# Performance work log

Measured on AMD Instinct MI355X. Metric: run time of the kernel, lower is better.

Reference implementation:

```python
import jax, jax.numpy as jnp
import numpy as np
from functools import partial

B = 131072          # training_size (batch)
D_IN = 100          # init_shape
H = 50              # neurons
T = 100             # dimTimes
DT = 0.01           # dt = 1/100
GAMMA = 0.05        # gamma = 1/20
I0 = 0.12


def setup_inputs() -> dict:
    key = jax.random.key(0)
    ks = jax.random.split(key, 7)
    s = lambda fan_in: 1.0 / np.sqrt(fan_in)
    return {
        "x": jax.random.normal(ks[0], (B, D_IN), dtype=jnp.float32),
        "W0": jax.random.uniform(ks[1], (H, D_IN), jnp.float32, -s(D_IN), s(D_IN)),
        "b0": jax.random.uniform(ks[2], (H,), jnp.float32, -s(D_IN), s(D_IN)),
        "W1": jax.random.uniform(ks[3], (H, H), jnp.float32, -s(H), s(H)),
        "b1": jax.random.uniform(ks[4], (H,), jnp.float32, -s(H), s(H)),
        "W2": jax.random.uniform(ks[5], (T - 1, H), jnp.float32, -s(H), s(H)),
        "b2": jax.random.uniform(ks[6], (T - 1,), jnp.float32, -s(H), s(H)),
    }


def reference(x, W0, b0, W1, b1, W2, b2):
    # 3-layer MLP: 100 -> 50 -> 50 -> 99
    h = jax.nn.relu(x @ W0.T + b0)
    h = jax.nn.relu(h @ W1.T + b1)
    out = h @ W2.T + b2                      # [B, T-1] growth rates per step

    # Euler recurrence: I[:,k] = I[:,k-1] + dt*(out[:,k-1]*I*(1-I) - gamma*I)
    i0 = jnp.full((x.shape[0],), I0, dtype=out.dtype)

    def step(I_prev, o_k):
        I_new = I_prev + DT * (o_k * I_prev * (1.0 - I_prev) - GAMMA * I_prev)
        return I_new, I_new

    _, I_rest = jax.lax.scan(step, i0, out.T)   # I_rest: [T-1, B]
    I = jnp.concatenate([i0[:, None], I_rest.T], axis=1)  # [B, T]
    return I
```

## Files before the change

kernel.cpp:

```cpp
#include <hip/hip_runtime.h>
#include <stdint.h>

#define BB      131072
#define TT      100
#define DT_C    0.01f
#define GAMMA_C 0.05f
#define I0_C    0.12f

typedef short bf16x8 __attribute__((ext_vector_type(8)));
typedef float f32x4  __attribute__((ext_vector_type(4)));

#define F0_U16  0
#define F1_U16  (16*512)
#define F2_U16  (24*512)
#define NFRAG_U16 (38*512)

__device__ __forceinline__ uint16_t f2bf(float x) {
    uint32_t u = __builtin_bit_cast(uint32_t, x);
    return (uint16_t)((u + 0x7fffu + ((u >> 16) & 1u)) >> 16);
}

__device__ __forceinline__ uint32_t pk2(float a, float b) {
    return (uint32_t)f2bf(a) | ((uint32_t)f2bf(b) << 16);
}

__global__ void pack_kernel(const float* __restrict__ W0, const float* __restrict__ b0,
                            const float* __restrict__ W1, const float* __restrict__ b1,
                            const float* __restrict__ W2, const float* __restrict__ b2,
                            uint16_t* __restrict__ wsu)
{
    const int gid = blockIdx.x * blockDim.x + threadIdx.x;
    const int gsz = gridDim.x * blockDim.x;
    for (int idx = gid; idx < NFRAG_U16; idx += gsz) {
        int f = idx >> 9;
        int r = idx & 511;
        int L = r >> 3, j = r & 7;
        int k8 = ((L >> 4) << 3) + j;
        int n16 = L & 15;
        float v = 0.0f;
        if (f < 16) {
            int kc = f >> 2, nt = f & 3;
            int kk = kc * 32 + k8, nn = nt * 16 + n16;
            if (nn < 50) {
                if (kk < 100) v = W0[nn * 100 + kk];
                else if (kk == 100) v = b0[nn];
            }
        } else if (f < 24) {
            int g = f - 16; int kc = g >> 2, nt = g & 3;
            int kk = kc * 32 + k8, nn = nt * 16 + n16;
            if (nn < 50) {
                if (kk < 50) v = W1[nn * 50 + kk];
                else if (kk == 50) v = b1[nn];
            }
        } else {
            int g = f - 24; int kc = g / 7, nt = g % 7;
            int kk = kc * 32 + k8, nn = nt * 16 + n16;
            if (nn < 99) {
                if (kk < 50) v = DT_C * W2[nn * 50 + kk];
                else if (kk == 50) v = DT_C * b2[nn];
            }
        }
        wsu[idx] = f2bf(v);
    }
}

#define SLAB_F 3712

__global__ __launch_bounds__(256, 2) void net_kernel(
    const float* __restrict__ x,
    const void*  __restrict__ wsv,
    float* __restrict__ out)
{
    __shared__ float lds[4 * SLAB_F];
    const int tid  = threadIdx.x;
    const int wave = tid >> 6, lane = tid & 63;
    const int quad = lane >> 4, l15 = lane & 15;
    float* slabF = lds + wave * SLAB_F;
    uint16_t* h0u = (uint16_t*)slabF;
    uint16_t* h1u = (uint16_t*)slabF + 32 * 88;
    const uint16_t* wsu = (const uint16_t*)wsv;

    const int row0 = (blockIdx.x * 4 + wave) * 32;

    bf16x8 a0[2][4];
    #pragma unroll
    for (int h = 0; h < 2; ++h) {
        const float* xrow = x + (size_t)(row0 + h * 16 + l15) * 100;
        #pragma unroll
        for (int kc = 0; kc < 3; ++kc) {
            f32x4 p = *(const f32x4*)(xrow + kc * 32 + quad * 8);
            f32x4 q = *(const f32x4*)(xrow + kc * 32 + quad * 8 + 4);
            union { bf16x8 v; uint32_t u[4]; } t;
            t.u[0] = pk2(p[0], p[1]); t.u[1] = pk2(p[2], p[3]);
            t.u[2] = pk2(q[0], q[1]); t.u[3] = pk2(q[2], q[3]);
            a0[h][kc] = t.v;
        }
        union { bf16x8 v; uint32_t u[4]; } t;
        t.u[0] = t.u[1] = t.u[2] = t.u[3] = 0u;
        if (quad == 0) {
            f32x4 p = *(const f32x4*)(xrow + 96);
            t.u[0] = pk2(p[0], p[1]); t.u[1] = pk2(p[2], p[3]);
            t.u[2] = 0x00003f80u;
        }
        a0[h][3] = t.v;
    }

    f32x4 acc0[2][4];
    #pragma unroll
    for (int h = 0; h < 2; ++h)
        #pragma unroll
        for (int nt = 0; nt < 4; ++nt) acc0[h][nt] = (f32x4){0.f, 0.f, 0.f, 0.f};
    #pragma unroll
    for (int kc = 0; kc < 4; ++kc) {
        #pragma unroll
        for (int nt = 0; nt < 4; ++nt) {
            bf16x8 b = ((const bf16x8*)(wsu + F0_U16 + (kc * 4 + nt) * 512))[lane];
            acc0[0][nt] = __builtin_amdgcn_mfma_f32_16x16x32_bf16(a0[0][kc], b, acc0[0][nt], 0, 0, 0);
            acc0[1][nt] = __builtin_amdgcn_mfma_f32_16x16x32_bf16(a0[1][kc], b, acc0[1][nt], 0, 0, 0);
        }
    }
    const bool is50 = (l15 == 2);
    #pragma unroll
    for (int h = 0; h < 2; ++h) {
        #pragma unroll
        for (int nt = 0; nt < 4; ++nt) {
            const int n = nt * 16 + l15;
            #pragma unroll
            for (int r2 = 0; r2 < 4; r2 += 2) {
                float v0 = fmaxf(acc0[h][nt][r2], 0.0f);
                float v1 = fmaxf(acc0[h][nt][r2 + 1], 0.0f);
                if (nt == 3 && is50) { v0 = 1.0f; v1 = 1.0f; }
                uint32_t p = pk2(v0, v1);
                const int m = h * 16 + quad * 4 + r2;
                h0u[m * 88 + n]       = (uint16_t)p;
                h0u[(m + 1) * 88 + n] = (uint16_t)(p >> 16);
            }
        }
    }

    bf16x8 a1[2][2];
    #pragma unroll
    for (int h = 0; h < 2; ++h)
        #pragma unroll
        for (int kc = 0; kc < 2; ++kc)
            a1[h][kc] = *(const bf16x8*)(h0u + (h * 16 + l15) * 88 + kc * 32 + quad * 8);

    f32x4 acc1[2][4];
    #pragma unroll
    for (int h = 0; h < 2; ++h)
        #pragma unroll
        for (int nt = 0; nt < 4; ++nt) acc1[h][nt] = (f32x4){0.f, 0.f, 0.f, 0.f};
    #pragma unroll
    for (int kc = 0; kc < 2; ++kc) {
        #pragma unroll
        for (int nt = 0; nt < 4; ++nt) {
            bf16x8 b = ((const bf16x8*)(wsu + F1_U16 + (kc * 4 + nt) * 512))[lane];
            acc1[0][nt] = __builtin_amdgcn_mfma_f32_16x16x32_bf16(a1[0][kc], b, acc1[0][nt], 0, 0, 0);
            acc1[1][nt] = __builtin_amdgcn_mfma_f32_16x16x32_bf16(a1[1][kc], b, acc1[1][nt], 0, 0, 0);
        }
    }
    #pragma unroll
    for (int h = 0; h < 2; ++h) {
        #pragma unroll
        for (int nt = 0; nt < 4; ++nt) {
            const int n = nt * 16 + l15;
            #pragma unroll
            for (int r2 = 0; r2 < 4; r2 += 2) {
                float v0 = fmaxf(acc1[h][nt][r2], 0.0f);
                float v1 = fmaxf(acc1[h][nt][r2 + 1], 0.0f);
                if (nt == 3 && is50) { v0 = 1.0f; v1 = 1.0f; }
                uint32_t p = pk2(v0, v1);
                const int m = h * 16 + quad * 4 + r2;
                h1u[m * 88 + n]       = (uint16_t)p;
                h1u[(m + 1) * 88 + n] = (uint16_t)(p >> 16);
            }
        }
    }

    bf16x8 a2[2][2];
    #pragma unroll
    for (int h = 0; h < 2; ++h)
        #pragma unroll
        for (int kc = 0; kc < 2; ++kc)
            a2[h][kc] = *(const bf16x8*)(h1u + (h * 16 + l15) * 88 + kc * 32 + quad * 8);

    f32x4 acc2[2][7];
    #pragma unroll
    for (int h = 0; h < 2; ++h)
        #pragma unroll
        for (int nt = 0; nt < 7; ++nt) acc2[h][nt] = (f32x4){0.f, 0.f, 0.f, 0.f};
    #pragma unroll
    for (int kc = 0; kc < 2; ++kc) {
        #pragma unroll
        for (int nt = 0; nt < 7; ++nt) {
            bf16x8 b = ((const bf16x8*)(wsu + F2_U16 + (kc * 7 + nt) * 512))[lane];
            acc2[0][nt] = __builtin_amdgcn_mfma_f32_16x16x32_bf16(a2[0][kc], b, acc2[0][nt], 0, 0, 0);
            acc2[1][nt] = __builtin_amdgcn_mfma_f32_16x16x32_bf16(a2[1][kc], b, acc2[1][nt], 0, 0, 0);
        }
    }
    #pragma unroll
    for (int h = 0; h < 2; ++h) {
        #pragma unroll
        for (int nt = 0; nt < 7; ++nt) {
            const int t = nt * 16 + l15;
            #pragma unroll
            for (int r = 0; r < 4; ++r)
                slabF[(h * 16 + quad * 4 + r) * 116 + t] = acc2[h][nt][r];
        }
    }

    if (lane < 32) {
        float* orow = slabF + lane * 116;
        float prev = I0_C;
        #pragma unroll
        for (int k = 1; k < TT; ++k) {
            const float op = orow[k - 1];
            orow[k - 1] = prev;
            prev = prev * fmaf(op, 1.0f - prev, 1.0f - DT_C * GAMMA_C);
        }
        orow[TT - 1] = prev;
    }

    float* gout = out + (size_t)row0 * 100;
    #pragma unroll
    for (int q = 0; q < 13; ++q) {
        const int i = q * 64 + lane;
        if (i < 800) {
            const int m = i / 25, c4 = (i % 25) * 4;
            f32x4 v = *(const f32x4*)(slabF + m * 116 + c4);
            *(f32x4*)(gout + 4 * i) = v;
        }
    }
}

extern "C" void kernel_launch(void* const* d_in, const int* in_sizes, int n_in,
                              void* d_out, int out_size, void* d_ws, size_t ws_size,
                              hipStream_t stream) {
    const float* x  = (const float*)d_in[0];
    const float* W0 = (const float*)d_in[1];
    const float* b0 = (const float*)d_in[2];
    const float* W1 = (const float*)d_in[3];
    const float* b1 = (const float*)d_in[4];
    const float* W2 = (const float*)d_in[5];
    const float* b2 = (const float*)d_in[6];
    float* out = (float*)d_out;
    uint16_t* wsu = (uint16_t*)d_ws;

    pack_kernel<<<dim3(80), dim3(256), 0, stream>>>(W0, b0, W1, b1, W2, b2, wsu);
    net_kernel<<<dim3(BB / 128), dim3(256), 0, stream>>>(x, (const void*)wsu, out);
}
```

Measured before the change: 123.6 us.

## Halve rows per wave and write recurrence output directly to global memory

Each wave now handles 16 rows instead of 32, which halves the LDS slab and the register footprint. Launch bounds are raised to 4 blocks per SM and the grid is doubled. The Euler recurrence now reads four outputs at a time from LDS and writes float4 results straight to global memory, removing the LDS writeback and the separate cooperative store loop. The trade-off is that only 16 lanes perform the serial recurrence and the global stores are per-row strided instead of coalesced across the wave.

```diff
diff --git a/kernel.cpp b/kernel.cpp
--- a/kernel.cpp
+++ b/kernel.cpp
@@ -19,7 +19,6 @@
     uint32_t u = __builtin_bit_cast(uint32_t, x);
     return (uint16_t)((u + 0x7fffu + ((u >> 16) & 1u)) >> 16);
 }
-
 __device__ __forceinline__ uint32_t pk2(float a, float b) {
     return (uint32_t)f2bf(a) | ((uint32_t)f2bf(b) << 16);
 }
@@ -64,9 +63,9 @@
     }
 }
 
-#define SLAB_F 3712
-
-__global__ __launch_bounds__(256, 2) void net_kernel(
+#define SLAB_F 1856
+
+__global__ __launch_bounds__(256, 4) void net_kernel(
     const float* __restrict__ x,
     const void*  __restrict__ wsv,
     float* __restrict__ out)
@@ -77,15 +76,14 @@
     const int quad = lane >> 4, l15 = lane & 15;
     float* slabF = lds + wave * SLAB_F;
     uint16_t* h0u = (uint16_t*)slabF;
-    uint16_t* h1u = (uint16_t*)slabF + 32 * 88;
+    uint16_t* h1u = (uint16_t*)slabF + 16 * 88;
     const uint16_t* wsu = (const uint16_t*)wsv;
 
-    const int row0 = (blockIdx.x * 4 + wave) * 32;
-
-    bf16x8 a0[2][4];
-    #pragma unroll
-    for (int h = 0; h < 2; ++h) {
-        const float* xrow = x + (size_t)(row0 + h * 16 + l15) * 100;
+    const int row0 = (blockIdx.x * 4 + wave) * 16;
+
+    bf16x8 a0[4];
+    {
+        const float* xrow = x + (size_t)(row0 + l15) * 100;
         #pragma unroll
         for (int kc = 0; kc < 3; ++kc) {
             f32x4 p = *(const f32x4*)(xrow + kc * 32 + quad * 8);
@@ -93,7 +91,7 @@
             union { bf16x8 v; uint32_t u[4]; } t;
             t.u[0] = pk2(p[0], p[1]); t.u[1] = pk2(p[2], p[3]);
             t.u[2] = pk2(q[0], q[1]); t.u[3] = pk2(q[2], q[3]);
-            a0[h][kc] = t.v;
+            a0[kc] = t.v;
         }
         union { bf16x8 v; uint32_t u[4]; } t;
         t.u[0] = t.u[1] = t.u[2] = t.u[3] = 0u;
@@ -102,133 +100,105 @@
             t.u[0] = pk2(p[0], p[1]); t.u[1] = pk2(p[2], p[3]);
             t.u[2] = 0x00003f80u;
         }
-        a0[h][3] = t.v;
-    }
-
-    f32x4 acc0[2][4];
-    #pragma unroll
-    for (int h = 0; h < 2; ++h)
-        #pragma unroll
-        for (int nt = 0; nt < 4; ++nt) acc0[h][nt] = (f32x4){0.f, 0.f, 0.f, 0.f};
+        a0[3] = t.v;
+    }
+
+    f32x4 acc0[4];
+    #pragma unroll
+    for (int nt = 0; nt < 4; ++nt) acc0[nt] = (f32x4){0.f, 0.f, 0.f, 0.f};
     #pragma unroll
     for (int kc = 0; kc < 4; ++kc) {
         #pragma unroll
         for (int nt = 0; nt < 4; ++nt) {
             bf16x8 b = ((const bf16x8*)(wsu + F0_U16 + (kc * 4 + nt) * 512))[lane];
-            acc0[0][nt] = __builtin_amdgcn_mfma_f32_16x16x32_bf16(a0[0][kc], b, acc0[0][nt], 0, 0, 0);
-            acc0[1][nt] = __builtin_amdgcn_mfma_f32_16x16x32_bf16(a0[1][kc], b, acc0[1][nt], 0, 0, 0);
+            acc0[nt] = __builtin_amdgcn_mfma_f32_16x16x32_bf16(a0[kc], b, acc0[nt], 0, 0, 0);
         }
     }
     const bool is50 = (l15 == 2);
     #pragma unroll
-    for (int h = 0; h < 2; ++h) {
-        #pragma unroll
-        for (int nt = 0; nt < 4; ++nt) {
-            const int n = nt * 16 + l15;
-            #pragma unroll
-            for (int r2 = 0; r2 < 4; r2 += 2) {
-                float v0 = fmaxf(acc0[h][nt][r2], 0.0f);
-                float v1 = fmaxf(acc0[h][nt][r2 + 1], 0.0f);
-                if (nt == 3 && is50) { v0 = 1.0f; v1 = 1.0f; }
-                uint32_t p = pk2(v0, v1);
-                const int m = h * 16 + quad * 4 + r2;
-                h0u[m * 88 + n]       = (uint16_t)p;
-                h0u[(m + 1) * 88 + n] = (uint16_t)(p >> 16);
-            }
-        }
-    }
-
-    bf16x8 a1[2][2];
-    #pragma unroll
-    for (int h = 0; h < 2; ++h)
-        #pragma unroll
-        for (int kc = 0; kc < 2; ++kc)
-            a1[h][kc] = *(const bf16x8*)(h0u + (h * 16 + l15) * 88 + kc * 32 + quad * 8);
-
-    f32x4 acc1[2][4];
-    #pragma unroll
-    for (int h = 0; h < 2; ++h)
-        #pragma unroll
-        for (int nt = 0; nt < 4; ++nt) acc1[h][nt] = (f32x4){0.f, 0.f, 0.f, 0.f};
+    for (int nt = 0; nt < 4; ++nt) {
+        const int n = nt * 16 + l15;
+        #pragma unroll
+        for (int r2 = 0; r2 < 4; r2 += 2) {
+            float v0 = fmaxf(acc0[nt][r2], 0.0f);
+            float v1 = fmaxf(acc0[nt][r2 + 1], 0.0f);
+            if (nt == 3 && is50) { v0 = 1.0f; v1 = 1.0f; }
+            uint32_t p = pk2(v0, v1);
+            const int m = quad * 4 + r2;
+            h0u[m * 88 + n]       = (uint16_t)p;
+            h0u[(m + 1) * 88 + n] = (uint16_t)(p >> 16);
+        }
+    }
+
+    bf16x8 a1[2];
+    #pragma unroll
+    for (int kc = 0; kc < 2; ++kc)
+        a1[kc] = *(const bf16x8*)(h0u + l15 * 88 + kc * 32 + quad * 8);
+
+    f32x4 acc1[4];
+    #pragma unroll
+    for (int nt = 0; nt < 4; ++nt) acc1[nt] = (f32x4){0.f, 0.f, 0.f, 0.f};
     #pragma unroll
     for (int kc = 0; kc < 2; ++kc) {
         #pragma unroll
         for (int nt = 0; nt < 4; ++nt) {
             bf16x8 b = ((const bf16x8*)(wsu + F1_U16 + (kc * 4 + nt) * 512))[lane];
-            acc1[0][nt] = __builtin_amdgcn_mfma_f32_16x16x32_bf16(a1[0][kc], b, acc1[0][nt], 0, 0, 0);
-            acc1[1][nt] = __builtin_amdgcn_mfma_f32_16x16x32_bf16(a1[1][kc], b, acc1[1][nt], 0, 0, 0);
-        }
-    }
-    #pragma unroll
-    for (int h = 0; h < 2; ++h) {
-        #pragma unroll
-        for (int nt = 0; nt < 4; ++nt) {
-            const int n = nt * 16 + l15;
-            #pragma unroll
-            for (int r2 = 0; r2 < 4; r2 += 2) {
-                float v0 = fmaxf(acc1[h][nt][r2], 0.0f);
-                float v1 = fmaxf(acc1[h][nt][r2 + 1], 0.0f);
-                if (nt == 3 && is50) { v0 = 1.0f; v1 = 1.0f; }
-                uint32_t p = pk2(v0, v1);
-                const int m = h * 16 + quad * 4 + r2;
-                h1u[m * 88 + n]       = (uint16_t)p;
-                h1u[(m + 1) * 88 + n] = (uint16_t)(p >> 16);
-            }
-        }
-    }
-
-    bf16x8 a2[2][2];
-    #pragma unroll
-    for (int h = 0; h < 2; ++h)
-        #pragma unroll
-        for (int kc = 0; kc < 2; ++kc)
-            a2[h][kc] = *(const bf16x8*)(h1u + (h * 16 + l15) * 88 + kc * 32 + quad * 8);
-
-    f32x4 acc2[2][7];
-    #pragma unroll
-    for (int h = 0; h < 2; ++h)
-        #pragma unroll
-        for (int nt = 0; nt < 7; ++nt) acc2[h][nt] = (f32x4){0.f, 0.f, 0.f, 0.f};
+            acc1[nt] = __builtin_amdgcn_mfma_f32_16x16x32_bf16(a1[kc], b, acc1[nt], 0, 0, 0);
+        }
+    }
+    #pragma unroll
+    for (int nt = 0; nt < 4; ++nt) {
+        const int n = nt * 16 + l15;
+        #pragma unroll
+        for (int r2 = 0; r2 < 4; r2 += 2) {
+            float v0 = fmaxf(acc1[nt][r2], 0.0f);
+            float v1 = fmaxf(acc1[nt][r2 + 1], 0.0f);
+            if (nt == 3 && is50) { v0 = 1.0f; v1 = 1.0f; }
+            uint32_t p = pk2(v0, v1);
+            const int m = quad * 4 + r2;
+            h1u[m * 88 + n]       = (uint16_t)p;
+            h1u[(m + 1) * 88 + n] = (uint16_t)(p >> 16);
+        }
+    }
+
+    bf16x8 a2[2];
+    #pragma unroll
+    for (int kc = 0; kc < 2; ++kc)
+        a2[kc] = *(const bf16x8*)(h1u + l15 * 88 + kc * 32 + quad * 8);
+
+    f32x4 acc2[7];
+    #pragma unroll
+    for (int nt = 0; nt < 7; ++nt) acc2[nt] = (f32x4){0.f, 0.f, 0.f, 0.f};
     #pragma unroll
     for (int kc = 0; kc < 2; ++kc) {
         #pragma unroll
         for (int nt = 0; nt < 7; ++nt) {
             bf16x8 b = ((const bf16x8*)(wsu + F2_U16 + (kc * 7 + nt) * 512))[lane];
-            acc2[0][nt] = __builtin_amdgcn_mfma_f32_16x16x32_bf16(a2[0][kc], b, acc2[0][nt], 0, 0, 0);
-            acc2[1][nt] = __builtin_amdgcn_mfma_f32_16x16x32_bf16(a2[1][kc], b, acc2[1][nt], 0, 0, 0);
-        }
-    }
-    #pragma unroll
-    for (int h = 0; h < 2; ++h) {
-        #pragma unroll
-        for (int nt = 0; nt < 7; ++nt) {
-            const int t = nt * 16 + l15;
-            #pragma unroll
-            for (int r = 0; r < 4; ++r)
-                slabF[(h * 16 + quad * 4 + r) * 116 + t] = acc2[h][nt][r];
-        }
-    }
-
-    if (lane < 32) {
-        float* orow = slabF + lane * 116;
+            acc2[nt] = __builtin_amdgcn_mfma_f32_16x16x32_bf16(a2[kc], b, acc2[nt], 0, 0, 0);
+        }
+    }
+    #pragma unroll
+    for (int nt = 0; nt < 7; ++nt) {
+        const int t = nt * 16 + l15;
+        #pragma unroll
+        for (int r = 0; r < 4; ++r)
+            slabF[(quad * 4 + r) * 116 + t] = acc2[nt][r];
+    }
+
+    if (lane < 16) {
+        const f32x4* orow4 = (const f32x4*)(slabF + lane * 116);
+        f32x4* gout = (f32x4*)(out + (size_t)(row0 + lane) * 100);
         float prev = I0_C;
         #pragma unroll
-        for (int k = 1; k < TT; ++k) {
-            const float op = orow[k - 1];
-            orow[k - 1] = prev;
-            prev = prev * fmaf(op, 1.0f - prev, 1.0f - DT_C * GAMMA_C);
-        }
-        orow[TT - 1] = prev;
-    }
-
-    float* gout = out + (size_t)row0 * 100;
-    #pragma unroll
-    for (int q = 0; q < 13; ++q) {
-        const int i = q * 64 + lane;
-        if (i < 800) {
-            const int m = i / 25, c4 = (i % 25) * 4;
-            f32x4 v = *(const f32x4*)(slabF + m * 116 + c4);
-            *(f32x4*)(gout + 4 * i) = v;
+        for (int c = 0; c < 25; ++c) {
+            const f32x4 o = orow4[c];
+            f32x4 v;
+            v.x = prev;
+            v.y = prev * fmaf(o[0], 1.0f - prev, 1.0f - DT_C * GAMMA_C); prev = v.y;
+            v.z = prev * fmaf(o[1], 1.0f - prev, 1.0f - DT_C * GAMMA_C); prev = v.z;
+            v.w = prev * fmaf(o[2], 1.0f - prev, 1.0f - DT_C * GAMMA_C); prev = v.w;
+            gout[c] = v;
+            prev = prev * fmaf(o[3], 1.0f - prev, 1.0f - DT_C * GAMMA_C);
         }
     }
 }
@@ -247,5 +217,5 @@
     uint16_t* wsu = (uint16_t*)d_ws;
 
     pack_kernel<<<dim3(80), dim3(256), 0, stream>>>(W0, b0, W1, b1, W2, b2, wsu);
-    net_kernel<<<dim3(BB / 128), dim3(256), 0, stream>>>(x, (const void*)wsu, out);
-}
+    net_kernel<<<dim3(BB / 64), dim3(256), 0, stream>>>(x, (const void*)wsu, out);
+}
```

After: 131.3 us. 6.2% more time.
